# Kernel optimization log

Measured on AMD Instinct MI355X. Metric: run time of the kernel, lower is better.

Reference implementation:

```python
import jax, jax.numpy as jnp
import numpy as np

NEG_SLOPE = 0.2

def _leaky_relu(x):
    return jnp.where(x >= 0, x, NEG_SLOPE * x)


def setup_inputs() -> dict:
    key = jax.random.key(0)
    ks = jax.random.split(key, 8)
    n_s, n_t, nnz = 100000, 20000, 2000000
    d_s_in, d_t_in, d_s_out, d_t_out = 128, 128, 64, 64
    # xavier-uniform-like scale (gain=1.414)
    def xav(k, shape):
        fan_in, fan_out = shape[0], shape[1]
        lim = 1.414 * np.sqrt(6.0 / (fan_in + fan_out))
        return jax.random.uniform(k, shape, jnp.float32, -lim, lim)
    return {
        "x_source": jax.random.normal(ks[0], (n_s, d_s_in), jnp.float32),
        "x_target": jax.random.normal(ks[1], (n_t, d_t_in), jnp.float32),
        "nbhd_values": jax.random.uniform(ks[2], (nnz,), jnp.float32),
        "w_s": xav(ks[3], (d_s_in, d_t_out)),
        "w_t": xav(ks[4], (d_t_in, d_s_out)),
        "att_weight": xav(ks[5], (d_t_out + d_s_out, 1)),
        "row_idx": jax.random.randint(ks[6], (nnz,), 0, n_t),  # target rows of N
        "col_idx": jax.random.randint(ks[7], (nnz,), 0, n_s),  # source cols of N
    }


def reference(x_source, x_target, nbhd_values, w_s, w_t, att_weight, row_idx, col_idx):
    n_s = x_source.shape[0]
    n_t = x_target.shape[0]
    d_t_out = w_s.shape[1]

    s_msg = x_source @ w_s  # [n_s, target_out]
    t_msg = x_target @ w_t  # [n_t, source_out]

    # att_weight applies to concat([s_msg_j, t_msg_i]); split it per-node
    a_s = att_weight[:d_t_out, 0]   # matches s_msg dims
    a_t = att_weight[d_t_out:, 0]   # matches t_msg dims
    s_score = s_msg @ a_s           # [n_s]
    t_score = t_msg @ a_t           # [n_t]

    # per-edge unnormalized attention; identical value for e (N-shaped) and
    # f (N^T-shaped) since concat order + swapped att vector cancel out
    edge = _leaky_relu(s_score[col_idx] + t_score[row_idx])  # [nnz]

    # sparse_row_norm: divide each row by its sum (rows of N for e, rows of N^T for f)
    e_row_sum = jax.ops.segment_sum(edge, row_idx, num_segments=n_t)
    f_row_sum = jax.ops.segment_sum(edge, col_idx, num_segments=n_s)
    e_att = edge / jnp.where(e_row_sum == 0, 1.0, e_row_sum)[row_idx]
    f_att = edge / jnp.where(f_row_sum == 0, 1.0, f_row_sum)[col_idx]

    # Hadamard with neighborhood values, then sparse-dense matmul (scatter-add)
    e_vals = e_att * nbhd_values  # (N \odot A_s) values
    f_vals = f_att * nbhd_values  # (N^T \odot A_t) values
    message_on_target = jax.ops.segment_sum(e_vals[:, None] * s_msg[col_idx], row_idx, num_segments=n_t)
    message_on_source = jax.ops.segment_sum(f_vals[:, None] * t_msg[row_idx], col_idx, num_segments=n_s)

    # update_func=None -> identity
    return message_on_source, message_on_target
```

## Files before the change

kernel.cpp:

```cpp
#include <hip/hip_runtime.h>
#include <stdint.h>

#define D_IN  128
#define D_OUT 64
#define NEG_SLOPE 0.2f
#define SUB       8
#define SUB_SHIFT 3
#define SCAN_CHUNK 4096
#define RPW       8
#define RPB       32

#define CHUNK   3072
#define UPT     12
#define GS_R    5
#define GS_C    7
#define CAPB_R  3712
#define CAPB_C  3072

__global__ void msg_score8_kernel(const float* __restrict__ x,
                                  const float* __restrict__ w,
                                  const float* __restrict__ att, int att_off,
                                  float* __restrict__ msg,
                                  float* __restrict__ score,
                                  int n_rows) {
    __shared__ float wl[D_IN * D_OUT];
    __shared__ float xs[RPB * D_IN];
    const int tid = threadIdx.x;

    const float4* w4  = (const float4*)w;
    float4*       wl4 = (float4*)wl;
#pragma unroll
    for (int i = 0; i < 8; ++i) wl4[tid + i * 256] = w4[tid + i * 256];

    const int rb = blockIdx.x * RPB;
    float4* xs4 = (float4*)xs;
    const float4* x4 = (const float4*)x;
#pragma unroll
    for (int i = 0; i < 4; ++i) {
        const int f  = tid + i * 256;
        const int r  = f >> 5;
        const int k4 = f & 31;
        const int row = min(rb + r, n_rows - 1);
        xs4[f] = x4[(size_t)row * 32 + k4];
    }
    __syncthreads();

    const int wv = tid >> 6;
    const int j  = tid & 63;
    const int rl = wv * RPW;
    const float4* xw = (const float4*)(xs + rl * D_IN);

    float acc[RPW];
#pragma unroll
    for (int r = 0; r < RPW; ++r) acc[r] = 0.f;

#pragma unroll 2
    for (int k4 = 0; k4 < D_IN / 4; ++k4) {
        const float w0 = wl[(k4 * 4 + 0) * D_OUT + j];
        const float w1 = wl[(k4 * 4 + 1) * D_OUT + j];
        const float w2 = wl[(k4 * 4 + 2) * D_OUT + j];
        const float w3 = wl[(k4 * 4 + 3) * D_OUT + j];
#pragma unroll
        for (int r = 0; r < RPW; ++r) {
            const float4 xv = xw[r * 32 + k4];
            acc[r] += xv.x * w0;
            acc[r] += xv.y * w1;
            acc[r] += xv.z * w2;
            acc[r] += xv.w * w3;
        }
    }

    const float aj = att[att_off + j];
#pragma unroll
    for (int r = 0; r < RPW; ++r) {
        const int row = rb + rl + r;
        if (row < n_rows) msg[(size_t)row * D_OUT + j] = acc[r];
        float v = acc[r] * aj;
#pragma unroll
        for (int off = 32; off > 0; off >>= 1) v += __shfl_down(v, off, 64);
        if (j == 0 && row < n_rows) score[row] = v;
    }
}

__global__ void __launch_bounds__(256)
khist2_kernel(const int* __restrict__ row_idx, const int* __restrict__ col_idx,
              int* __restrict__ cntR, int* __restrict__ cntC,
              int nnz, int ngr, int ngc) {
    extern __shared__ int hs[];
    int* hr = hs;
    int* hc = hs + ngr;
    const int tid  = threadIdx.x;
    const int base = blockIdx.x * CHUNK;
    const int lim  = min(CHUNK, nnz - base);

    for (int k = tid; k < ngr + ngc; k += 256) hs[k] = 0;
    __syncthreads();
    for (int k = tid; k < lim; k += 256) {
        atomicAdd(&hr[row_idx[base + k] >> GS_R], 1);
        atomicAdd(&hc[col_idx[base + k] >> GS_C], 1);
    }
    __syncthreads();
    for (int g = tid; g < ngr; g += 256) cntR[(size_t)blockIdx.x * ngr + g] = hr[g];
    for (int g = tid; g < ngc; g += 256) cntC[(size_t)blockIdx.x * ngc + g] = hc[g];
}

__global__ void __launch_bounds__(256)
kgsum_kernel(const int* __restrict__ cnt, int* __restrict__ gtot,
             int NB, int ng) {
    __shared__ int lds[256];
    const int g = blockIdx.x;
    const int t = threadIdx.x;
    int s = 0;
    for (int b = t; b < NB; b += 256) s += cnt[(size_t)b * ng + g];
    lds[t] = s;
    __syncthreads();
    for (int d = 128; d > 0; d >>= 1) {
        if (t < d) lds[t] += lds[t + d];
        __syncthreads();
    }
    if (t == 0) gtot[g] = lds[0];
}

__global__ void __launch_bounds__(1024)
kgscan2_kernel(const int* __restrict__ gtotR, int* __restrict__ goffR, int ngr,
               const int* __restrict__ gtotC, int* __restrict__ goffC, int ngc) {
    __shared__ int lds[1024];
    const int t = threadIdx.x;
    const int* gt = blockIdx.x ? gtotC : gtotR;
    int*       go = blockIdx.x ? goffC : goffR;
    const int  n  = blockIdx.x ? ngc : ngr;
    const int v = (t < n) ? gt[t] : 0;
    lds[t] = v;
    __syncthreads();
    for (int d = 1; d < 1024; d <<= 1) {
        int u = (t >= d) ? lds[t - d] : 0;
        __syncthreads();
        lds[t] += u;
        __syncthreads();
    }
    if (t < n) go[t] = lds[t] - v;
    if (t == n - 1) go[n] = lds[t];
}

__global__ void __launch_bounds__(256)
kgpos_kernel(const int* __restrict__ cnt, const int* __restrict__ goff,
             int* __restrict__ gpos, int NB, int ng) {
    __shared__ int lds[256];
    const int g = blockIdx.x;
    const int t = threadIdx.x;
    int c[3];
    int s = 0;
#pragma unroll
    for (int u = 0; u < 3; ++u) {
        const int b = 3 * t + u;
        c[u] = (b < NB) ? cnt[(size_t)b * ng + g] : 0;
        s += c[u];
    }
    lds[t] = s;
    __syncthreads();
    for (int d = 1; d < 256; d <<= 1) {
        int u = (t >= d) ? lds[t - d] : 0;
        __syncthreads();
        lds[t] += u;
        __syncthreads();
    }
    int ex = goff[g] + lds[t] - s;
#pragma unroll
    for (int u = 0; u < 3; ++u) {
        const int b = 3 * t + u;
        if (b < NB) { gpos[(size_t)g * NB + b] = ex; ex += c[u]; }
    }
}

__global__ void __launch_bounds__(256)
kpart3_kernel(const int* __restrict__ row_idx,
              const int* __restrict__ col_idx,
              const float* __restrict__ nbhd,
              const float* __restrict__ s_score,
              const float* __restrict__ t_score,
              const int* __restrict__ gposR, const int* __restrict__ gposC,
              float4* __restrict__ pay_r, float4* __restrict__ pay_c,
              int nnz, int NB, int ngr, int ngc) {
    extern __shared__ char sm[];
    float4* sp   = (float4*)sm;
    int*    cnt  = (int*)(sm + (size_t)CHUNK * 16);
    int*    off  = cnt + (ngc + 1);
    int*    gofb = off + (ngc + 1);

    const int tid  = threadIdx.x;
    const int b    = blockIdx.x;
    const int base = b * CHUNK;
    const int lim  = min(CHUNK, nnz - base);

    int   rr[UPT], cc[UPT];
    float ee[UPT], bb[UPT];
#pragma unroll
    for (int u = 0; u < UPT; ++u) {
        const int k = tid + u * 256;
        rr[u] = 0; cc[u] = 0; ee[u] = 0.f; bb[u] = 0.f;
        if (k < lim) {
            const int r = row_idx[base + k];
            const int c = col_idx[base + k];
            rr[u] = r; cc[u] = c; bb[u] = nbhd[base + k];
            const float xv = s_score[c] + t_score[r];
            ee[u] = xv >= 0.f ? xv : NEG_SLOPE * xv;
        }
    }

#pragma unroll 1
    for (int d = 0; d < 2; ++d) {
        const int gs   = d ? GS_C : GS_R;
        const int ng   = d ? ngc : ngr;
        const int mask = (1 << gs) - 1;
        const int* gp  = d ? gposC : gposR;
        float4*    pd  = d ? pay_c : pay_r;

        for (int k = tid; k <= ng; k += 256) cnt[k] = 0;
        __syncthreads();

#pragma unroll
        for (int u = 0; u < UPT; ++u) {
            const int k = tid + u * 256;
            if (k < lim) atomicAdd(&cnt[(d ? cc[u] : rr[u]) >> gs], 1);
        }
        __syncthreads();

        if (tid == 0) {
            int a = 0;
            for (int k = 0; k < ng; ++k) { const int t = cnt[k]; off[k] = a; cnt[k] = a; a += t; }
            off[ng] = a;
        }
        __syncthreads();

        for (int k = tid; k < ng; k += 256) gofb[k] = gp[(size_t)k * NB + b];

#pragma unroll
        for (int u = 0; u < UPT; ++u) {
            const int k = tid + u * 256;
            if (k < lim) {
                const int key = d ? cc[u] : rr[u];
                const int oth = d ? rr[u] : cc[u];
                const int grp = key >> gs;
                const int pos = atomicAdd(&cnt[grp], 1);
                sp[pos] = make_float4(__int_as_float(oth | ((key & mask) << 20)),
                                      ee[u], bb[u], __int_as_float(grp));
            }
        }
        __syncthreads();

        for (int k = tid; k < lim; k += 256) {
            const float4 p = sp[k];
            const int grp = __float_as_int(p.w);
            pd[(size_t)gofb[grp] + (k - off[grp])] = p;
        }
        __syncthreads();
    }
}

__global__ void __launch_bounds__(512)
ksort_kernel(float4* __restrict__ pay,
             const int* __restrict__ goff,
             int* __restrict__ koff,
             int kpg, int cap) {
    extern __shared__ char sm[];
    int*    PO   = (int*)sm;
    float*  E    = (float*)(sm + (size_t)cap * 4);
    float*  B    = (float*)(sm + (size_t)cap * 8);
    unsigned short* perm = (unsigned short*)(sm + (size_t)cap * 12);
    int*    scnt = (int*)(sm + (size_t)cap * 14);
    int*    soff = scnt + kpg;
    int*    scur = soff + kpg + 1;

    const int g    = blockIdx.x;
    const int tid  = threadIdx.x;
    const int mask = kpg - 1;

    const int beg = goff[g];
    const int n   = min(goff[g + 1] - beg, cap);

    for (int k = tid; k < kpg; k += 512) scnt[k] = 0;
    __syncthreads();

    for (int k = tid; k < n; k += 512) {
        const float4 p = pay[(size_t)beg + k];
        const int pk = __float_as_int(p.x);
        PO[k] = pk; E[k] = p.y; B[k] = p.z;
        atomicAdd(&scnt[(pk >> 20) & mask], 1);
    }
    __syncthreads();

    if (tid == 0) {
        int a = 0;
        for (int k = 0; k < kpg; ++k) { const int t = scnt[k]; soff[k] = a; scur[k] = a; a += t; }
        soff[kpg] = a;
    }
    __syncthreads();

    for (int k = tid; k < n; k += 512)
        perm[atomicAdd(&scur[(PO[k] >> 20) & mask], 1)] = (unsigned short)k;
    __syncthreads();

    for (int k = tid; k < n; k += 512) {
        const int kk = perm[k];
        pay[(size_t)beg + k] = make_float4(__int_as_float(PO[kk]), E[kk], B[kk], 0.f);
    }
    for (int k = tid; k <= kpg; k += 512)
        koff[(size_t)g * (kpg + 1) + k] = beg + soff[k];
}

__global__ void kaccum2_kernel(const int* __restrict__ koff, int kshift,
                               const float4* __restrict__ pay,
                               const float* __restrict__ other_msg,
                               float* __restrict__ out, int n_mine) {
    const int wave = (int)((blockIdx.x * (size_t)blockDim.x + threadIdx.x) >> 6);
    const int lane = threadIdx.x & 63;
    if (wave >= n_mine) return;

    const int kpg = 1 << kshift;
    const int grp = wave >> kshift;
    const int jk  = wave & (kpg - 1);
    const int beg = koff[(size_t)grp * (kpg + 1) + jk];
    const int end = koff[(size_t)grp * (kpg + 1) + jk + 1];

    double psum = 0.0;
    for (int k = beg + lane; k < end; k += 64) psum += (double)pay[k].y;
#pragma unroll
    for (int o = 32; o > 0; o >>= 1) psum += __shfl_down(psum, o, 64);
    double ers = __shfl(psum, 0, 64);
    if (ers == 0.0) ers = 1.0;
    const double inv = 1.0 / ers;

    const int g = lane >> 4;
    const int q = lane & 15;
    const float4* msg4 = (const float4*)other_msg;
    float4 acc = make_float4(0.f, 0.f, 0.f, 0.f);

    for (int kb = beg; kb < end; kb += 64) {
        const int k = kb + lane;
        int o = 0; float wt = 0.f;
        if (k < end) {
            float4 p = pay[k];
            o  = __float_as_int(p.x) & 0xFFFFF;
            wt = (float)((double)p.y * inv) * p.z;
        }
        const int cnt = min(64, end - kb);
        for (int j = 0; j < cnt; j += 4) {
            const int   jj = j + g;
            const int   oj = __shfl(o,  jj, 64);
            const float wj = __shfl(wt, jj, 64);
            float4 m = msg4[((size_t)oj << 4) + q];
            acc.x += wj * m.x;
            acc.y += wj * m.y;
            acc.z += wj * m.z;
            acc.w += wj * m.w;
        }
    }

#pragma unroll
    for (int d = 16; d < 64; d <<= 1) {
        acc.x += __shfl_xor(acc.x, d, 64);
        acc.y += __shfl_xor(acc.y, d, 64);
        acc.z += __shfl_xor(acc.z, d, 64);
        acc.w += __shfl_xor(acc.w, d, 64);
    }
    if (g == 0) ((float4*)out)[((size_t)wave << 4) + q] = acc;
}

__global__ void hist_kernel(const int* __restrict__ row_idx,
                            const int* __restrict__ col_idx,
                            int* __restrict__ cnt, int col_base, int nnz) {
    const int i = blockIdx.x * blockDim.x + threadIdx.x;
    if (i >= nnz) return;
    const int s = i & (SUB - 1);
    atomicAdd(&cnt[(row_idx[i] << SUB_SHIFT) + s], 1);
    atomicAdd(&cnt[col_base + (col_idx[i] << SUB_SHIFT) + s], 1);
}

__global__ void scan_stage1(const int* __restrict__ cnt, int* __restrict__ bsum,
                            int n) {
    __shared__ int lds[256];
    const int t = threadIdx.x;
    const int base = blockIdx.x * SCAN_CHUNK;
    int s = 0;
    for (int k = t; k < SCAN_CHUNK; k += 256) {
        const int j = base + k;
        if (j < n) s += cnt[j];
    }
    lds[t] = s;
    __syncthreads();
    for (int d = 128; d > 0; d >>= 1) {
        if (t < d) lds[t] += lds[t + d];
        __syncthreads();
    }
    if (t == 0) bsum[blockIdx.x] = lds[0];
}

__global__ void scan_stage2(int* __restrict__ bsum, int nb) {
    __shared__ int lds[1024];
    const int t = threadIdx.x;
    const int v = (t < nb) ? bsum[t] : 0;
    lds[t] = v;
    __syncthreads();
    for (int d = 1; d < 1024; d <<= 1) {
        int u = (t >= d) ? lds[t - d] : 0;
        __syncthreads();
        lds[t] += u;
        __syncthreads();
    }
    if (t < nb) bsum[t] = lds[t] - v;
}

__global__ void scan_stage3(const int* __restrict__ cnt,
                            const int* __restrict__ bsum,
                            int* __restrict__ off, int* __restrict__ cur,
                            int n, int total) {
    __shared__ int lds[256];
    const int t = threadIdx.x;
    const int base = blockIdx.x * SCAN_CHUNK + t * 16;
    int c[16];
    int s = 0;
#pragma unroll
    for (int k = 0; k < 16; ++k) {
        const int j = base + k;
        c[k] = (j < n) ? cnt[j] : 0;
        s += c[k];
    }
    lds[t] = s;
    __syncthreads();
    for (int d = 1; d < 256; d <<= 1) {
        int u = (t >= d) ? lds[t - d] : 0;
        __syncthreads();
        lds[t] += u;
        __syncthreads();
    }
    int ex = bsum[blockIdx.x] + lds[t] - s;
#pragma unroll
    for (int k = 0; k < 16; ++k) {
        const int j = base + k;
        if (j < n) { off[j] = ex; cur[j] = ex; ex += c[k]; }
    }
    if (blockIdx.x == 0 && t == 0) off[n] = total;
}

__global__ void scatter_row_kernel(const int* __restrict__ row_idx,
                                   const int* __restrict__ col_idx,
                                   const float* __restrict__ nbhd,
                                   const float* __restrict__ s_score,
                                   const float* __restrict__ t_score,
                                   int* __restrict__ cur,
                                   float4* __restrict__ pay, int nnz) {
    const int i = blockIdx.x * blockDim.x + threadIdx.x;
    if (i >= nnz) return;
    const int r = row_idx[i];
    const int c = col_idx[i];
    const float xv = s_score[c] + t_score[r];
    const float e  = xv >= 0.f ? xv : NEG_SLOPE * xv;
    const int p = atomicAdd(&cur[(r << SUB_SHIFT) + (i & (SUB - 1))], 1);
    pay[p] = make_float4(__int_as_float(c), e, nbhd[i], 0.f);
}

__global__ void scatter_col_kernel(const int* __restrict__ row_idx,
                                   const int* __restrict__ col_idx,
                                   const float* __restrict__ nbhd,
                                   const float* __restrict__ s_score,
                                   const float* __restrict__ t_score,
                                   int* __restrict__ cur, int col_base,
                                   float4* __restrict__ pay, int nnz) {
    const int i = blockIdx.x * blockDim.x + threadIdx.x;
    if (i >= nnz) return;
    const int r = row_idx[i];
    const int c = col_idx[i];
    const float xv = s_score[c] + t_score[r];
    const float e  = xv >= 0.f ? xv : NEG_SLOPE * xv;
    const int p = atomicAdd(&cur[col_base + (c << SUB_SHIFT) + (i & (SUB - 1))], 1);
    pay[p] = make_float4(__int_as_float(r), e, nbhd[i], 0.f);
}

__global__ void accum_kernel(const int* __restrict__ off, int off_base,
                             const float4* __restrict__ pay,
                             const float* __restrict__ other_msg,
                             float* __restrict__ out, int n_mine) {
    const int wave = (int)((blockIdx.x * (size_t)blockDim.x + threadIdx.x) >> 6);
    const int lane = threadIdx.x & 63;
    if (wave >= n_mine) return;

    const int beg = off[off_base + (wave << SUB_SHIFT)];
    const int end = off[off_base + (wave << SUB_SHIFT) + SUB];

    double psum = 0.0;
    for (int k = beg + lane; k < end; k += 64) psum += (double)pay[k].y;
#pragma unroll
    for (int o = 32; o > 0; o >>= 1) psum += __shfl_down(psum, o, 64);
    double ers = __shfl(psum, 0, 64);
    if (ers == 0.0) ers = 1.0;
    const double inv = 1.0 / ers;

    const int g = lane >> 4;
    const int q = lane & 15;
    const float4* msg4 = (const float4*)other_msg;
    float4 acc = make_float4(0.f, 0.f, 0.f, 0.f);

    for (int kb = beg; kb < end; kb += 64) {
        const int k = kb + lane;
        int o = 0; float wt = 0.f;
        if (k < end) {
            float4 p = pay[k];
            o  = __float_as_int(p.x);
            wt = (float)((double)p.y * inv) * p.z;
        }
        const int cnt = min(64, end - kb);
        for (int j = 0; j < cnt; j += 4) {
            const int   jj = j + g;
            const int   oj = __shfl(o,  jj, 64);
            const float wj = __shfl(wt, jj, 64);
            float4 m = msg4[((size_t)oj << 4) + q];
            acc.x += wj * m.x;
            acc.y += wj * m.y;
            acc.z += wj * m.z;
            acc.w += wj * m.w;
        }
    }

#pragma unroll
    for (int d = 16; d < 64; d <<= 1) {
        acc.x += __shfl_xor(acc.x, d, 64);
        acc.y += __shfl_xor(acc.y, d, 64);
        acc.z += __shfl_xor(acc.z, d, 64);
        acc.w += __shfl_xor(acc.w, d, 64);
    }
    if (g == 0) ((float4*)out)[((size_t)wave << 4) + q] = acc;
}

extern "C" void kernel_launch(void* const* d_in, const int* in_sizes, int n_in,
                              void* d_out, int out_size, void* d_ws, size_t ws_size,
                              hipStream_t stream) {
    const float* x_source = (const float*)d_in[0];
    const float* x_target = (const float*)d_in[1];
    const float* nbhd     = (const float*)d_in[2];
    const float* w_s      = (const float*)d_in[3];
    const float* w_t      = (const float*)d_in[4];
    const float* att      = (const float*)d_in[5];
    const int*   row_idx  = (const int*)d_in[6];
    const int*   col_idx  = (const int*)d_in[7];

    const int n_s = in_sizes[0] / D_IN;
    const int n_t = in_sizes[1] / D_IN;
    const int nnz = in_sizes[2];

    float* out = (float*)d_out;
    float* mos = out;
    float* mot = out + (size_t)n_s * D_OUT;

    char* ws = (char*)d_ws;
    float* s_msg   = (float*)ws;  ws += sizeof(float) * (size_t)n_s * D_OUT;
    float* t_msg   = (float*)ws;  ws += sizeof(float) * (size_t)n_t * D_OUT;
    float* s_score = (float*)ws;  ws += sizeof(float) * (size_t)n_s;
    float* t_score = (float*)ws;  ws += sizeof(float) * (size_t)n_t;

    const int NBCH = (nnz + CHUNK - 1) / CHUNK;
    const int NGR  = (n_t + (1 << GS_R) - 1) >> GS_R;
    const int NGC  = (n_s + (1 << GS_C) - 1) >> GS_C;
    char* wsb = ws;
    int* cntR  = (int*)wsb;  wsb += sizeof(int) * (size_t)NBCH * NGR;
    int* cntC  = (int*)wsb;  wsb += sizeof(int) * (size_t)NBCH * NGC;
    int* gposR = (int*)wsb;  wsb += sizeof(int) * (size_t)NGR * NBCH;
    int* gposC = (int*)wsb;  wsb += sizeof(int) * (size_t)NGC * NBCH;
    int* gtotR = (int*)wsb;  wsb += sizeof(int) * (size_t)NGR;
    int* goffR = (int*)wsb;  wsb += sizeof(int) * (size_t)(NGR + 1);
    int* gtotC = (int*)wsb;  wsb += sizeof(int) * (size_t)NGC;
    int* goffC = (int*)wsb;  wsb += sizeof(int) * (size_t)(NGC + 1);
    int* koffR = (int*)wsb;  wsb += sizeof(int) * (size_t)NGR * ((1 << GS_R) + 1);
    int* koffC = (int*)wsb;  wsb += sizeof(int) * (size_t)NGC * ((1 << GS_C) + 1);
    wsb = (char*)(((uintptr_t)wsb + 15) & ~(uintptr_t)15);
    float4* pay_r = (float4*)wsb;  wsb += sizeof(float4) * (size_t)nnz;
    float4* pay_c = (float4*)wsb;  wsb += sizeof(float4) * (size_t)nnz;
    const size_t need_sort = (size_t)(wsb - (char*)d_ws);

    msg_score8_kernel<<<(n_s + RPB - 1) / RPB, 256, 0, stream>>>(
        x_source, w_s, att, 0, s_msg, s_score, n_s);
    msg_score8_kernel<<<(n_t + RPB - 1) / RPB, 256, 0, stream>>>(
        x_target, w_t, att, D_OUT, t_msg, t_score, n_t);

    if (ws_size >= need_sort) {
        khist2_kernel<<<NBCH, 256, (size_t)(NGR + NGC) * 4, stream>>>(
            row_idx, col_idx, cntR, cntC, nnz, NGR, NGC);

        kgsum_kernel<<<NGR, 256, 0, stream>>>(cntR, gtotR, NBCH, NGR);
        kgsum_kernel<<<NGC, 256, 0, stream>>>(cntC, gtotC, NBCH, NGC);
        kgscan2_kernel<<<2, 1024, 0, stream>>>(gtotR, goffR, NGR, gtotC, goffC, NGC);
        kgpos_kernel<<<NGR, 256, 0, stream>>>(cntR, goffR, gposR, NBCH, NGR);
        kgpos_kernel<<<NGC, 256, 0, stream>>>(cntC, goffC, gposC, NBCH, NGC);

        const size_t smem_part = (size_t)CHUNK * 16 + (size_t)(3 * (NGC + 1)) * 4;
        kpart3_kernel<<<NBCH, 256, smem_part, stream>>>(
            row_idx, col_idx, nbhd, s_score, t_score,
            gposR, gposC, pay_r, pay_c, nnz, NBCH, NGR, NGC);

        const size_t smem_s_r = (size_t)CAPB_R * 14 + (size_t)(3 * (1 << GS_R) + 2) * 4;
        const size_t smem_s_c = (size_t)CAPB_C * 14 + (size_t)(3 * (1 << GS_C) + 2) * 4;
        ksort_kernel<<<NGR, 512, smem_s_r, stream>>>(
            pay_r, goffR, koffR, 1 << GS_R, CAPB_R);
        ksort_kernel<<<NGC, 512, smem_s_c, stream>>>(
            pay_c, goffC, koffC, 1 << GS_C, CAPB_C);

        kaccum2_kernel<<<(int)(((size_t)n_t * 64 + 255) / 256), 256, 0, stream>>>(
            koffR, GS_R, pay_r, s_msg, mot, n_t);
        kaccum2_kernel<<<(int)(((size_t)n_s * 64 + 255) / 256), 256, 0, stream>>>(
            koffC, GS_C, pay_c, t_msg, mos, n_s);
    } else {
        const int col_base = n_t * SUB;
        const int n_cnt    = (n_t + n_s) * SUB;
        const int total    = 2 * nnz;

        char* wsf = ws;
        int* cnt  = (int*)wsf;  wsf += sizeof(int) * (size_t)n_cnt;
        int* cur  = (int*)wsf;  wsf += sizeof(int) * (size_t)n_cnt;
        int* off  = (int*)wsf;  wsf += sizeof(int) * (size_t)(n_cnt + 1);
        int* bsum = (int*)wsf;  wsf += sizeof(int) * 1024;
        wsf = (char*)(((uintptr_t)wsf + 15) & ~(uintptr_t)15);
        float4* pay = (float4*)wsf;

        hipMemsetAsync(cnt, 0, sizeof(int) * (size_t)n_cnt, stream);

        hist_kernel<<<(nnz + 255) / 256, 256, 0, stream>>>(
            row_idx, col_idx, cnt, col_base, nnz);

        const int nb = (n_cnt + SCAN_CHUNK - 1) / SCAN_CHUNK;
        scan_stage1<<<nb, 256, 0, stream>>>(cnt, bsum, n_cnt);
        scan_stage2<<<1, 1024, 0, stream>>>(bsum, nb);
        scan_stage3<<<nb, 256, 0, stream>>>(cnt, bsum, off, cur, n_cnt, total);

        scatter_row_kernel<<<(nnz + 255) / 256, 256, 0, stream>>>(
            row_idx, col_idx, nbhd, s_score, t_score, cur, pay, nnz);
        scatter_col_kernel<<<(nnz + 255) / 256, 256, 0, stream>>>(
            row_idx, col_idx, nbhd, s_score, t_score, cur, col_base, pay, nnz);

        accum_kernel<<<(int)(((size_t)n_t * 64 + 255) / 256), 256, 0, stream>>>(
            off, 0, pay, s_msg, mot, n_t);
        accum_kernel<<<(int)(((size_t)n_s * 64 + 255) / 256), 256, 0, stream>>>(
            off, col_base, pay, t_msg, mos, n_s);
    }
}
```

Measured before the change: 529.3 us.

## Shrink partition chunk, drop register staging, parallelize group offset scan

```diff
diff --git a/kernel.cpp b/kernel.cpp
--- a/kernel.cpp
+++ b/kernel.cpp
@@ -10,8 +10,7 @@
 #define RPW       8
 #define RPB       32
 
-#define CHUNK   3072
-#define UPT     12
+#define CHUNK   2048
 #define GS_R    5
 #define GS_C    7
 #define CAPB_R  3712
@@ -148,11 +147,11 @@
     __shared__ int lds[256];
     const int g = blockIdx.x;
     const int t = threadIdx.x;
-    int c[3];
+    int c[4];
     int s = 0;
 #pragma unroll
-    for (int u = 0; u < 3; ++u) {
-        const int b = 3 * t + u;
+    for (int u = 0; u < 4; ++u) {
+        const int b = 4 * t + u;
         c[u] = (b < NB) ? cnt[(size_t)b * ng + g] : 0;
         s += c[u];
     }
@@ -166,8 +165,8 @@
     }
     int ex = goff[g] + lds[t] - s;
 #pragma unroll
-    for (int u = 0; u < 3; ++u) {
-        const int b = 3 * t + u;
+    for (int u = 0; u < 4; ++u) {
+        const int b = 4 * t + u;
         if (b < NB) { gpos[(size_t)g * NB + b] = ex; ex += c[u]; }
     }
 }
@@ -192,59 +191,61 @@
     const int base = b * CHUNK;
     const int lim  = min(CHUNK, nnz - base);
 
-    int   rr[UPT], cc[UPT];
-    float ee[UPT], bb[UPT];
-#pragma unroll
-    for (int u = 0; u < UPT; ++u) {
-        const int k = tid + u * 256;
-        rr[u] = 0; cc[u] = 0; ee[u] = 0.f; bb[u] = 0.f;
-        if (k < lim) {
-            const int r = row_idx[base + k];
-            const int c = col_idx[base + k];
-            rr[u] = r; cc[u] = c; bb[u] = nbhd[base + k];
-            const float xv = s_score[c] + t_score[r];
-            ee[u] = xv >= 0.f ? xv : NEG_SLOPE * xv;
-        }
-    }
-
 #pragma unroll 1
     for (int d = 0; d < 2; ++d) {
         const int gs   = d ? GS_C : GS_R;
         const int ng   = d ? ngc : ngr;
         const int mask = (1 << gs) - 1;
+        const int* kidx = d ? col_idx : row_idx;
+        const int* oidx = d ? row_idx : col_idx;
         const int* gp  = d ? gposC : gposR;
         float4*    pd  = d ? pay_c : pay_r;
 
         for (int k = tid; k <= ng; k += 256) cnt[k] = 0;
         __syncthreads();
 
-#pragma unroll
-        for (int u = 0; u < UPT; ++u) {
-            const int k = tid + u * 256;
-            if (k < lim) atomicAdd(&cnt[(d ? cc[u] : rr[u]) >> gs], 1);
-        }
-        __syncthreads();
-
-        if (tid == 0) {
-            int a = 0;
-            for (int k = 0; k < ng; ++k) { const int t = cnt[k]; off[k] = a; cnt[k] = a; a += t; }
-            off[ng] = a;
+        for (int k = tid; k < lim; k += 256)
+            atomicAdd(&cnt[kidx[base + k] >> gs], 1);
+        __syncthreads();
+
+        const int ipt = (ng + 1 + 255) >> 8;
+        int c4[4];
+        int s = 0;
+#pragma unroll
+        for (int u = 0; u < 4; ++u) {
+            const int k = tid * ipt + u;
+            c4[u] = (u < ipt && k <= ng) ? cnt[k] : 0;
+            s += c4[u];
+        }
+        gofb[tid] = s;
+        __syncthreads();
+        for (int dd = 1; dd < 256; dd <<= 1) {
+            const int uu = (tid >= dd) ? gofb[tid - dd] : 0;
+            __syncthreads();
+            gofb[tid] += uu;
+            __syncthreads();
+        }
+        int ex = gofb[tid] - s;
+        __syncthreads();
+#pragma unroll
+        for (int u = 0; u < 4; ++u) {
+            const int k = tid * ipt + u;
+            if (u < ipt && k <= ng) { off[k] = ex; cnt[k] = ex; ex += c4[u]; }
         }
         __syncthreads();
 
         for (int k = tid; k < ng; k += 256) gofb[k] = gp[(size_t)k * NB + b];
-
-#pragma unroll
-        for (int u = 0; u < UPT; ++u) {
-            const int k = tid + u * 256;
-            if (k < lim) {
-                const int key = d ? cc[u] : rr[u];
-                const int oth = d ? rr[u] : cc[u];
-                const int grp = key >> gs;
-                const int pos = atomicAdd(&cnt[grp], 1);
-                sp[pos] = make_float4(__int_as_float(oth | ((key & mask) << 20)),
-                                      ee[u], bb[u], __int_as_float(grp));
-            }
+        for (int k = tid; k < lim; k += 256) {
+            const int key = kidx[base + k];
+            const int oth = oidx[base + k];
+            const int r   = d ? oth : key;
+            const int c   = d ? key : oth;
+            const float xv = s_score[c] + t_score[r];
+            const float e  = xv >= 0.f ? xv : NEG_SLOPE * xv;
+            const int grp = key >> gs;
+            const int pos = atomicAdd(&cnt[grp], 1);
+            sp[pos] = make_float4(__int_as_float(oth | ((key & mask) << 20)),
+                                  e, nbhd[base + k], __int_as_float(grp));
         }
         __syncthreads();
 
@@ -591,7 +592,7 @@
         kgpos_kernel<<<NGR, 256, 0, stream>>>(cntR, goffR, gposR, NBCH, NGR);
         kgpos_kernel<<<NGC, 256, 0, stream>>>(cntC, goffC, gposC, NBCH, NGC);
 
-        const size_t smem_part = (size_t)CHUNK * 16 + (size_t)(3 * (NGC + 1)) * 4;
+        const size_t smem_part = (size_t)CHUNK * 16 + (size_t)(3 * NGC + 2) * 4;
         kpart3_kernel<<<NBCH, 256, smem_part, stream>>>(
             row_idx, col_idx, nbhd, s_score, t_score,
             gposR, gposC, pay_r, pay_c, nnz, NBCH, NGR, NGC);
```

Measured after the change: 483.4 us. -8.7%, faster.
